# Optimization experiments

Hardware: AMD Instinct MI355X
Metric: run time of the kernel (lower is better)

The kernel has to match this reference:

```python
import jax, jax.numpy as jnp
import numpy as np

B, NTX, S, OFDM, FFT = 16, 1, 4, 14, 1024   # batch, num_tx, streams, ofdm symbols, subcarriers
NRX, NRXA, T = 4, 1, 16                      # num_rx, rx antennas each, tx antennas


def setup_inputs() -> dict:
    key = jax.random.key(0)
    k = jax.random.split(key, 4)
    return {
        "x_real": jax.random.normal(k[0], (B, NTX, S, OFDM, FFT), jnp.float32),
        "x_imag": jax.random.normal(k[1], (B, NTX, S, OFDM, FFT), jnp.float32),
        "h_real": jax.random.normal(k[2], (B, NRX, NRXA, NTX, T, OFDM, FFT), jnp.float32),
        "h_imag": jax.random.normal(k[3], (B, NRX, NRXA, NTX, T, OFDM, FFT), jnp.float32),
        "precoding_ind": jnp.arange(S, dtype=jnp.int32),  # rx index per stream
    }


def _zero_forcing(x, h):
    # x: [..., S], h: [..., S, T]
    h_herm = jnp.conj(jnp.swapaxes(h, -1, -2))          # [..., T, S]
    hh_herm = jnp.matmul(h, h_herm)                     # [..., S, S] (tiny Gram matrix)
    g = jnp.matmul(h_herm, jnp.linalg.inv(hh_herm))     # [..., T, S] ZF precoder
    x_precoded = jnp.matmul(g, x[..., None])[..., 0]    # [..., T]
    return x_precoded, g


def reference(x_real, x_imag, h_real, h_imag, precoding_ind):
    x = (x_real + 1j * x_imag).astype(jnp.complex64)    # [B, NTX, S, OFDM, FFT]
    h = (h_real + 1j * h_imag).astype(jnp.complex64)    # [B, NRX, NRXA, NTX, T, OFDM, FFT]

    # x.permute(0,1,3,4,2): streams last
    x_p = jnp.transpose(x, (0, 1, 3, 4, 2))             # [B, NTX, OFDM, FFT, S]

    # h.permute(3,1,2,4,5,6,0)
    h_pc = jnp.transpose(h, (3, 1, 2, 4, 5, 6, 0))      # [NTX, NRX, NRXA, T, OFDM, FFT, B]
    # gather desired receivers along num_rx axis
    h_des = h_pc[:, precoding_ind]                      # [NTX, S, NRXA, T, OFDM, FFT, B]
    sh = h_des.shape
    # flatten_dims(., 2, 3): merge rx_ant into tx_ant axis (NRXA=1)
    h_des = h_des.reshape(sh[0], sh[1], sh[2] * sh[3], sh[4], sh[5], sh[6])
    # permute(5,0,3,4,1,2)
    h_des = jnp.transpose(h_des, (5, 0, 3, 4, 1, 2))    # [B, NTX, OFDM, FFT, S, T]

    x_precoded, g = _zero_forcing(x_p, h_des)           # [B, NTX, OFDM, FFT, T]
    # permute(0,1,4,2,3)
    return jnp.transpose(x_precoded, (0, 1, 4, 2, 3))   # [B, NTX, T, OFDM, FFT]
```

## Files before the change

### kernel.cpp

```cpp
#include <hip/hip_runtime.h>
#include <hip/hip_bf16.h>

#define NB    16
#define NS    4
#define NT    16
#define NOFDM 14
#define NFFT  1024
#define SITE  (NOFDM * NFFT)
#define NSITES (NB * SITE)

__device__ __forceinline__ unsigned short bf16_bits(float f) {
    unsigned int u = __float_as_uint(f);
    return (unsigned short)((u + 0x7FFFu + ((u >> 16) & 1u)) >> 16);
}

template <int MODE>
__global__ __launch_bounds__(256) void zf_precoder_kernel(
    const float* __restrict__ xr, const float* __restrict__ xi,
    const float* __restrict__ hr, const float* __restrict__ hi,
    void* __restrict__ out_raw)
{
    const int gid = blockIdx.x * 256 + threadIdx.x;
    if (gid >= NSITES) return;
    const int b   = gid / SITE;
    const int rem = gid - b * SITE;

    float Xr[NS], Xi[NS];
    const int xbase = b * (NS * SITE) + rem;
    #pragma unroll
    for (int s = 0; s < NS; ++s) {
        Xr[s] = xr[xbase + s * SITE];
        Xi[s] = xi[xbase + s * SITE];
    }

    float Hr[NS][NT], Hi[NS][NT];
    const int hbase = b * (NS * NT * SITE) + rem;
    #pragma unroll
    for (int s = 0; s < NS; ++s) {
        #pragma unroll
        for (int t = 0; t < NT; ++t) {
            const int idx = hbase + (s * NT + t) * SITE;
            Hr[s][t] = hr[idx];
            Hi[s][t] = hi[idx];
        }
    }

    float Ar[NS][NS], Ai[NS][NS];
    #pragma unroll
    for (int i = 0; i < NS; ++i) {
        #pragma unroll
        for (int j = 0; j <= i; ++j) {
            float sr = 0.f, si = 0.f;
            #pragma unroll
            for (int t = 0; t < NT; ++t) {
                sr += Hr[i][t] * Hr[j][t] + Hi[i][t] * Hi[j][t];
                si += Hi[i][t] * Hr[j][t] - Hr[i][t] * Hi[j][t];
            }
            Ar[i][j] = sr;
            Ai[i][j] = si;
        }
    }

    float invd[NS];
    #pragma unroll
    for (int j = 0; j < NS; ++j) {
        float s = Ar[j][j];
        #pragma unroll
        for (int k = 0; k < j; ++k)
            s -= Ar[j][k] * Ar[j][k] + Ai[j][k] * Ai[j][k];
        const float inv = 1.0f / sqrtf(fmaxf(s, 1e-20f));
        invd[j] = inv;
        #pragma unroll
        for (int i = j + 1; i < NS; ++i) {
            float sr = Ar[i][j], si = Ai[i][j];
            #pragma unroll
            for (int k = 0; k < j; ++k) {
                sr -= Ar[i][k] * Ar[j][k] + Ai[i][k] * Ai[j][k];
                si -= Ai[i][k] * Ar[j][k] - Ar[i][k] * Ai[j][k];
            }
            Ar[i][j] = sr * inv;
            Ai[i][j] = si * inv;
        }
    }

    float Wr[NS], Wi[NS];
    #pragma unroll
    for (int i = 0; i < NS; ++i) {
        float sr = Xr[i], si = Xi[i];
        #pragma unroll
        for (int k = 0; k < i; ++k) {
            sr -= Ar[i][k] * Wr[k] - Ai[i][k] * Wi[k];
            si -= Ar[i][k] * Wi[k] + Ai[i][k] * Wr[k];
        }
        Wr[i] = sr * invd[i];
        Wi[i] = si * invd[i];
    }

    float Zr[NS], Zi[NS];
    #pragma unroll
    for (int i = NS - 1; i >= 0; --i) {
        float sr = Wr[i], si = Wi[i];
        #pragma unroll
        for (int k = i + 1; k < NS; ++k) {
            sr -= Ar[k][i] * Zr[k] + Ai[k][i] * Zi[k];
            si -= Ar[k][i] * Zi[k] - Ai[k][i] * Zr[k];
        }
        Zr[i] = sr * invd[i];
        Zi[i] = si * invd[i];
    }

    const int obase = b * (NT * SITE) + rem;
    #pragma unroll
    for (int t = 0; t < NT; ++t) {
        float yr = 0.f, yi = 0.f;
        #pragma unroll
        for (int s = 0; s < NS; ++s) {
            yr += Hr[s][t] * Zr[s] + Hi[s][t] * Zi[s];
            yi += Hr[s][t] * Zi[s] - Hi[s][t] * Zr[s];
        }
        if (MODE == 0) {
            ((float*)out_raw)[obase + t * SITE] = yr;
        } else {
            ((unsigned int*)out_raw)[obase + t * SITE] =
                (unsigned int)bf16_bits(yr) | ((unsigned int)bf16_bits(yi) << 16);
        }
    }
}

extern "C" void kernel_launch(void* const* d_in, const int* in_sizes, int n_in,
                              void* d_out, int out_size, void* d_ws, size_t ws_size,
                              hipStream_t stream) {
    const float* xr = (const float*)d_in[0];
    const float* xi = (const float*)d_in[1];
    const float* hr = (const float*)d_in[2];
    const float* hi = (const float*)d_in[3];

    const int grid = (NSITES + 255) / 256;
    if (out_size == NB * NT * SITE) {
        zf_precoder_kernel<0><<<grid, 256, 0, stream>>>(xr, xi, hr, hi, d_out);
    } else {
        zf_precoder_kernel<1><<<grid, 256, 0, stream>>>(xr, xi, hr, hi, d_out);
    }
}
```

Before: 28.53 us.

## Split each site's tx antennas across four waves with LDS Gram reduction

Each site is now handled by four wavefronts, and each wave loads and processes 4 of the 16 tx antennas. Partial Gram matrices are summed through shared memory after a block barrier. Every wave then runs the Cholesky solve redundantly and writes its own 4 output antennas. This cuts per-thread registers and raises thread-level parallelism for a memory-bound kernel, at the cost of repeating the small solve four times and adding an LDS round trip plus a barrier. Launch bounds are also tightened to request at least two blocks per CU.

```diff
diff --git a/kernel.cpp b/kernel.cpp
--- a/kernel.cpp
+++ b/kernel.cpp
@@ -8,6 +8,7 @@
 #define NFFT  1024
 #define SITE  (NOFDM * NFFT)
 #define NSITES (NB * SITE)
+#define TPW   4
 
 __device__ __forceinline__ unsigned short bf16_bits(float f) {
     unsigned int u = __float_as_uint(f);
@@ -15,34 +16,37 @@
 }
 
 template <int MODE>
-__global__ __launch_bounds__(256) void zf_precoder_kernel(
+__global__ __launch_bounds__(256, 2)
+void zf_precoder_kernel(
     const float* __restrict__ xr, const float* __restrict__ xi,
     const float* __restrict__ hr, const float* __restrict__ hi,
     void* __restrict__ out_raw)
 {
-    const int gid = blockIdx.x * 256 + threadIdx.x;
-    if (gid >= NSITES) return;
-    const int b   = gid / SITE;
-    const int rem = gid - b * SITE;
+    const int tid  = threadIdx.x;
+    const int w    = tid >> 6;
+    const int l    = tid & 63;
+    const int site = blockIdx.x * 64 + l;
+    const int b    = site / SITE;
+    const int rem  = site - b * SITE;
+    const int t0   = w * TPW;
 
+    float Hr[NS][TPW], Hi[NS][TPW];
+    const int hbase = b * (NS * NT * SITE) + rem;
+    #pragma unroll
+    for (int s = 0; s < NS; ++s) {
+        #pragma unroll
+        for (int tt = 0; tt < TPW; ++tt) {
+            const int idx = hbase + (s * NT + t0 + tt) * SITE;
+            Hr[s][tt] = hr[idx];
+            Hi[s][tt] = hi[idx];
+        }
+    }
     float Xr[NS], Xi[NS];
     const int xbase = b * (NS * SITE) + rem;
     #pragma unroll
     for (int s = 0; s < NS; ++s) {
         Xr[s] = xr[xbase + s * SITE];
         Xi[s] = xi[xbase + s * SITE];
-    }
-
-    float Hr[NS][NT], Hi[NS][NT];
-    const int hbase = b * (NS * NT * SITE) + rem;
-    #pragma unroll
-    for (int s = 0; s < NS; ++s) {
-        #pragma unroll
-        for (int t = 0; t < NT; ++t) {
-            const int idx = hbase + (s * NT + t) * SITE;
-            Hr[s][t] = hr[idx];
-            Hi[s][t] = hi[idx];
-        }
     }
 
     float Ar[NS][NS], Ai[NS][NS];
@@ -52,13 +56,38 @@
         for (int j = 0; j <= i; ++j) {
             float sr = 0.f, si = 0.f;
             #pragma unroll
-            for (int t = 0; t < NT; ++t) {
-                sr += Hr[i][t] * Hr[j][t] + Hi[i][t] * Hi[j][t];
-                si += Hi[i][t] * Hr[j][t] - Hr[i][t] * Hi[j][t];
+            for (int tt = 0; tt < TPW; ++tt) {
+                sr += Hr[i][tt] * Hr[j][tt] + Hi[i][tt] * Hi[j][tt];
+                si += Hi[i][tt] * Hr[j][tt] - Hr[i][tt] * Hi[j][tt];
             }
             Ar[i][j] = sr;
             Ai[i][j] = si;
         }
+    }
+
+    __shared__ float lds[4 * 16 * 64];
+    {
+        float* p = &lds[(w * 16) * 64 + l];
+        p[ 0*64] = Ar[0][0]; p[ 1*64] = Ar[1][1]; p[ 2*64] = Ar[2][2]; p[ 3*64] = Ar[3][3];
+        p[ 4*64] = Ar[1][0]; p[ 5*64] = Ai[1][0];
+        p[ 6*64] = Ar[2][0]; p[ 7*64] = Ai[2][0];
+        p[ 8*64] = Ar[2][1]; p[ 9*64] = Ai[2][1];
+        p[10*64] = Ar[3][0]; p[11*64] = Ai[3][0];
+        p[12*64] = Ar[3][1]; p[13*64] = Ai[3][1];
+        p[14*64] = Ar[3][2]; p[15*64] = Ai[3][2];
+    }
+    __syncthreads();
+    #pragma unroll
+    for (int ow = 0; ow < 4; ++ow) {
+        if (ow == w) continue;
+        const float* p = &lds[(ow * 16) * 64 + l];
+        Ar[0][0] += p[ 0*64]; Ar[1][1] += p[ 1*64]; Ar[2][2] += p[ 2*64]; Ar[3][3] += p[ 3*64];
+        Ar[1][0] += p[ 4*64]; Ai[1][0] += p[ 5*64];
+        Ar[2][0] += p[ 6*64]; Ai[2][0] += p[ 7*64];
+        Ar[2][1] += p[ 8*64]; Ai[2][1] += p[ 9*64];
+        Ar[3][0] += p[10*64]; Ai[3][0] += p[11*64];
+        Ar[3][1] += p[12*64]; Ai[3][1] += p[13*64];
+        Ar[3][2] += p[14*64]; Ai[3][2] += p[15*64];
     }
 
     float invd[NS];
@@ -111,17 +140,18 @@
 
     const int obase = b * (NT * SITE) + rem;
     #pragma unroll
-    for (int t = 0; t < NT; ++t) {
+    for (int tt = 0; tt < TPW; ++tt) {
         float yr = 0.f, yi = 0.f;
         #pragma unroll
         for (int s = 0; s < NS; ++s) {
-            yr += Hr[s][t] * Zr[s] + Hi[s][t] * Zi[s];
-            yi += Hr[s][t] * Zi[s] - Hi[s][t] * Zr[s];
+            yr += Hr[s][tt] * Zr[s] + Hi[s][tt] * Zi[s];
+            yi += Hr[s][tt] * Zi[s] - Hi[s][tt] * Zr[s];
         }
+        const int o = obase + (t0 + tt) * SITE;
         if (MODE == 0) {
-            ((float*)out_raw)[obase + t * SITE] = yr;
+            ((float*)out_raw)[o] = yr;
         } else {
-            ((unsigned int*)out_raw)[obase + t * SITE] =
+            ((unsigned int*)out_raw)[o] =
                 (unsigned int)bf16_bits(yr) | ((unsigned int)bf16_bits(yi) << 16);
         }
     }
@@ -135,7 +165,7 @@
     const float* hr = (const float*)d_in[2];
     const float* hi = (const float*)d_in[3];
 
-    const int grid = (NSITES + 255) / 256;
+    const int grid = NSITES / 64;
     if (out_size == NB * NT * SITE) {
         zf_precoder_kernel<0><<<grid, 256, 0, stream>>>(xr, xi, hr, hi, d_out);
     } else {
```

New measurement: 28.68 us. About the same (+0.5%).
